# Kernel optimization log

Hardware: AMD Instinct MI355X
Metric: run time of the kernel (lower is better)

## Reference

```python
import jax, jax.numpy as jnp
import numpy as np

B, T, A, K, STEPS, E = 2, 16384, 128, 128, 16, 126


def soft_dirac_last(x):
    # softmax forward-replaced by one-hot(argmax), straight-through backward
    sm = jax.nn.softmax(x, axis=-1)
    hard = jax.nn.one_hot(jnp.argmax(x, axis=-1), x.shape[-1], dtype=x.dtype)
    return sm + jax.lax.stop_gradient(hard - sm)


def _encode(x, d_unit, atom_embeddings):
    # x: (B,1,T); d_unit: (A,K) unit-norm atoms
    rng = jnp.linspace(0.0, 1.0, T, dtype=x.dtype)
    kernel = d_unit[:, None, :]  # OIH
    pad = [(K // 2, K - 1 - K // 2)]  # SAME
    batch_ix = jnp.arange(B)

    def step(res, _):
        # dense feature map: correlation of residual with every atom
        fm = jax.lax.conv_general_dilated(
            res, kernel, window_strides=(1,), padding=pad,
            dimension_numbers=("NCH", "OIH", "NCH"))  # (B,A,T)
        flat = fm.reshape(B, A * T)
        fi = jnp.argmax(flat, axis=-1)                      # sparsify n_to_keep=1
        value = jnp.take_along_axis(flat, fi[:, None], axis=-1)  # (B,1)
        ai = fi // T
        ti = fi % T
        # position: soft_dirac over time of sparse fm summed over atoms
        pos_row = jnp.zeros((B, T), x.dtype).at[batch_ix, ti].set(value[:, 0])
        pd = soft_dirac_last(pos_row)
        position = jnp.sum(pd * rng[None, :], axis=-1, keepdims=True) * 20.0  # (B,1)
        # atom one-hot: soft_dirac over atom axis of sparse fm summed over time
        atom_row = jnp.zeros((B, A), x.dtype).at[batch_ix, ai].set(value[:, 0])
        ad = soft_dirac_last(atom_row)
        ae = ad @ atom_embeddings  # (B,E)
        emb = jnp.concatenate([position, value, ae], axis=-1)  # (B, 2+E)
        # matching-pursuit residual update: subtract value * atom at found shift
        recon = value * d_unit[ai]  # (B,K)
        buf = jnp.zeros((B, T + K), x.dtype)
        buf = jax.vmap(lambda bb, rr, tt: jax.lax.dynamic_update_slice(bb, rr, (tt,)))(buf, recon, ti)
        res = res - buf[:, None, K // 2:K // 2 + T]
        return res, emb

    res, embs = jax.lax.scan(step, x, None, length=STEPS)
    embs = jnp.transpose(embs, (1, 0, 2))  # (B, STEPS, 2+E)
    return embs, res


def _canonical_ordering(embs, proj):
    keys = embs @ proj  # (B, STEPS)
    order = jnp.argsort(keys, axis=-1)
    return jnp.take_along_axis(embs, order[:, :, None], axis=1)


def setup_inputs() -> dict:
    key = jax.random.key(0)
    ks = jax.random.split(key, 5)
    return {
        "a": jax.random.normal(ks[0], (B, 1, T), jnp.float32),
        "b": jax.random.normal(ks[1], (B, 1, T), jnp.float32),
        "d": jax.random.normal(ks[2], (A, K), jnp.float32),
        "atom_embeddings": jax.random.normal(ks[3], (A, E), jnp.float32) * 0.1,
        "ordering_proj": jax.random.normal(ks[4], (128,), jnp.float32),
    }


def reference(a, b, d, atom_embeddings, ordering_proj):
    d_unit = d / (jnp.linalg.norm(d, axis=-1, keepdims=True) + 1e-8)
    ae, a_res = _encode(a, d_unit, atom_embeddings)
    be, b_res = _encode(b, d_unit, atom_embeddings)
    ae = _canonical_ordering(ae, ordering_proj)
    be = _canonical_ordering(be, ordering_proj)
    a_norm = jnp.linalg.norm(a_res.reshape(-1, T), axis=-1)
    b_norm = jnp.linalg.norm(b_res.reshape(-1, T), axis=-1)
    return jnp.mean((ae - be) ** 2) + jnp.mean(jnp.abs(a_norm - b_norm))
```

## Files before the change

### kernel.cpp

```cpp
#include <hip/hip_runtime.h>
#include <math.h>

#define T_DIM 16384
#define A_DIM 128
#define K_DIM 128
#define N_STEPS 16
#define E_DIM 126
#define NSEQ 4

#define NPT0 512
#define NAT8 16
#define TT 256
#define NTT 64
#define HB 8192
#define RL_LEN 8319
#define SS_LEN 383
#define SPAD 16

#define PIDX(i) ((i) + ((i) >> 5))

#define NB_STEP0 (NPT0 * NSEQ)
#define NB_INC   (65 * NSEQ)
#define NB_TOTAL (NB_STEP0 + NB_INC + 1)

#define SM_U64 4448

__device__ inline unsigned long long pack_vi(float v, int fi) {
    unsigned int b = __float_as_uint(v);
    b = (b & 0x80000000u) ? ~b : (b | 0x80000000u);
    return ((unsigned long long)b << 32) | (unsigned int)(~fi);
}
__device__ inline void unpack_vi(unsigned long long p, float* v, int* fi) {
    unsigned int lo = (unsigned int)(p & 0xffffffffu);
    unsigned int b = (unsigned int)(p >> 32);
    unsigned int fb = (b & 0x80000000u) ? (b & 0x7fffffffu) : ~b;
    *v = __uint_as_float(fb);
    *fi = (int)(~lo);
}
__device__ inline unsigned long long u64max(unsigned long long a, unsigned long long b) {
    return a > b ? a : b;
}
__device__ inline unsigned long long pollu64(const unsigned long long* p) {
    unsigned long long v = __hip_atomic_load(p, __ATOMIC_RELAXED,
                                             __HIP_MEMORY_SCOPE_AGENT);
    while (v == 0ULL) {
        __builtin_amdgcn_s_sleep(1);
        v = __hip_atomic_load(p, __ATOMIC_RELAXED, __HIP_MEMORY_SCOPE_AGENT);
    }
    return v;
}

__global__ __launch_bounds__(256) void k_prep(
    const float* __restrict__ d, float* __restrict__ du,
    unsigned long long* __restrict__ arena) {
    int blk = blockIdx.x, tid = threadIdx.x;
    if (blk < 128) {
        __shared__ float s[128];
        float v = 0.0f;
        if (tid < 128) { v = d[blk * K_DIM + tid]; s[tid] = v * v; }
        __syncthreads();
        for (int off = 64; off > 0; off >>= 1) {
            if (tid < off) s[tid] += s[tid + off];
            __syncthreads();
        }
        if (tid < 128) du[blk * K_DIM + tid] = v / (sqrtf(s[0]) + 1e-8f);
    } else {
        int zb = blk - 128;
        for (int i = zb * 256 + tid; i < 31744; i += 64 * 256)
            arena[2048 + i] = 0ULL;
        if (blk == 128) {
            int* ctrl = (int*)(arena + 33792);
            if (tid < NSEQ) {
                ctrl[tid * 32] = 0;
                ((float*)ctrl)[160 + tid * 32] = 0.0f;
            }
            if (tid == 4) ctrl[128] = 0;
        }
    }
}

__device__ inline unsigned long long tile16(
    const float* __restrict__ duP, const float* __restrict__ rsh,
    int L0, int a_lo, int t_lo, int tid, unsigned long long* red4) {
    float acc[4][4];
    #pragma unroll
    for (int i = 0; i < 4; i++)
        #pragma unroll
        for (int j = 0; j < 4; j++) acc[i][j] = 0.0f;
    float r[8];
    #pragma unroll
    for (int m = 0; m < 8; m++) r[m] = rsh[PIDX(L0 + m)];
    #pragma unroll 4
    for (int k = 0; k < K_DIM; k += 4) {
        float dA[4][4];
        #pragma unroll
        for (int i = 0; i < 4; i++)
            *(float4*)dA[i] = *(const float4*)(duP + i * K_DIM + k);
        #pragma unroll
        for (int dk = 0; dk < 4; dk++) {
            #pragma unroll
            for (int i = 0; i < 4; i++) {
                float s = dA[i][dk];
                #pragma unroll
                for (int j = 0; j < 4; j++)
                    acc[i][j] = fmaf(s, r[j + dk], acc[i][j]);
            }
        }
        r[0] = r[4]; r[1] = r[5]; r[2] = r[6]; r[3] = r[7];
        #pragma unroll
        for (int m = 0; m < 4; m++) r[4 + m] = rsh[PIDX(L0 + k + 8 + m)];
    }
    float bv = -INFINITY;
    int bi = 0x7fffffff;
    #pragma unroll
    for (int i = 0; i < 4; i++) {
        int aa = a_lo + i;
        #pragma unroll
        for (int j = 0; j < 4; j++) {
            int fi = aa * T_DIM + t_lo + j;
            float v = acc[i][j];
            if (v > bv || (v == bv && fi < bi)) { bv = v; bi = fi; }
        }
    }
    #pragma unroll
    for (int off = 32; off > 0; off >>= 1) {
        float v2 = __shfl_down(bv, off);
        int   i2 = __shfl_down(bi, off);
        if (v2 > bv || (v2 == bv && i2 < bi)) { bv = v2; bi = i2; }
    }
    if ((tid & 63) == 0) red4[tid >> 6] = pack_vi(bv, bi);
    __syncthreads();
    if (tid == 0) {
        unsigned long long m = red4[0];
        #pragma unroll
        for (int w = 1; w < 4; w++) m = u64max(m, red4[w]);
        red4[0] = m;
    }
    __syncthreads();
    return red4[0];
}

__device__ inline unsigned long long tile8(
    const float* __restrict__ duP, const float* __restrict__ rsh,
    int L0, int a_lo, int t_lo, int tid, unsigned long long* red4) {
    float acc[2][4];
    #pragma unroll
    for (int i = 0; i < 2; i++)
        #pragma unroll
        for (int j = 0; j < 4; j++) acc[i][j] = 0.0f;
    float r[8];
    #pragma unroll
    for (int m = 0; m < 8; m++) r[m] = rsh[PIDX(L0 + m)];
    #pragma unroll 4
    for (int k = 0; k < K_DIM; k += 4) {
        float dA[2][4];
        #pragma unroll
        for (int i = 0; i < 2; i++)
            *(float4*)dA[i] = *(const float4*)(duP + i * K_DIM + k);
        #pragma unroll
        for (int dk = 0; dk < 4; dk++) {
            #pragma unroll
            for (int i = 0; i < 2; i++) {
                float s = dA[i][dk];
                #pragma unroll
                for (int j = 0; j < 4; j++)
                    acc[i][j] = fmaf(s, r[j + dk], acc[i][j]);
            }
        }
        r[0] = r[4]; r[1] = r[5]; r[2] = r[6]; r[3] = r[7];
        #pragma unroll
        for (int m = 0; m < 4; m++) r[4 + m] = rsh[PIDX(L0 + k + 8 + m)];
    }
    float bv = -INFINITY;
    int bi = 0x7fffffff;
    #pragma unroll
    for (int i = 0; i < 2; i++) {
        int aa = a_lo + i;
        #pragma unroll
        for (int j = 0; j < 4; j++) {
            int fi = aa * T_DIM + t_lo + j;
            float v = acc[i][j];
            if (v > bv || (v == bv && fi < bi)) { bv = v; bi = fi; }
        }
    }
    #pragma unroll
    for (int off = 32; off > 0; off >>= 1) {
        float v2 = __shfl_down(bv, off);
        int   i2 = __shfl_down(bi, off);
        if (v2 > bv || (v2 == bv && i2 < bi)) { bv = v2; bi = i2; }
    }
    if ((tid & 63) == 0) red4[tid >> 6] = pack_vi(bv, bi);
    __syncthreads();
    if (tid == 0) {
        unsigned long long m = red4[0];
        #pragma unroll
        for (int w = 1; w < 4; w++) m = u64max(m, red4[w]);
        red4[0] = m;
    }
    __syncthreads();
    return red4[0];
}

__global__ __launch_bounds__(256) void k_mega(
    const float* __restrict__ a, const float* __restrict__ b,
    const float* __restrict__ du, const float* __restrict__ ae,
    const float* __restrict__ proj, float* __restrict__ emb,
    unsigned long long* __restrict__ arena, float* __restrict__ out) {

    __shared__ unsigned long long SMEM[SM_U64];
    unsigned long long* pmax = arena;
    unsigned long long* dsl  = arena + 2048;
    unsigned long long* wsl  = arena + 32768;
    unsigned long long* w0   = arena + 33728;
    int*   cnt   = (int*)(arena + 33792);
    int*   done  = cnt + 128;
    float* norm2 = (float*)cnt + 160;

    int blk = blockIdx.x;
    int tid = threadIdx.x;

    if (blk < NB_STEP0) {
        int seq = blk >> 9;
        int idx = blk & 511;
        int a_base = (idx >> 6) * 16;
        int t0 = (idx & 63) * TT;
        float* rsh = (float*)SMEM;
        unsigned long long* pm_sh = SMEM + 256;
        unsigned long long* red4  = SMEM + 512;
        int* flag = (int*)(SMEM + 516);

        const float* x = (seq < 2 ? a : b) + (seq & 1) * T_DIM;
        for (int i = tid; i < SS_LEN; i += 256) {
            int t = t0 - 64 + i;
            rsh[PIDX(i)] = (t >= 0 && t < T_DIM) ? x[t] : 0.0f;
        }
        __syncthreads();
        int tg = tid & 63;
        int ag = __builtin_amdgcn_readfirstlane(tid >> 6);
        unsigned long long p = tile16(du + (a_base + ag * 4) * K_DIM, rsh,
                                      4 * tg, a_base + ag * 4, t0 + 4 * tg,
                                      tid, red4);
        if (tid == 0) {
            pmax[seq * NPT0 + idx] = p;
            __threadfence();
            flag[0] = (atomicAdd(&cnt[seq * 32], 1) == NPT0 - 1);
        }
        __syncthreads();
        if (!flag[0]) return;

        __threadfence();
        pm_sh[tid] = u64max(pmax[seq * NPT0 + tid], pmax[seq * NPT0 + 256 + tid]);
        __syncthreads();
        for (int off = 128; off > 0; off >>= 1) {
            if (tid < off) pm_sh[tid] = u64max(pm_sh[tid], pm_sh[tid + off]);
            __syncthreads();
        }
        float value; int fi;
        unpack_vi(pm_sh[0], &value, &fi);
        int ai = fi >> 14, ti = fi & (T_DIM - 1);
        int pos_idx = value > 0.0f ? ti : 0;
        int atom_idx = value > 0.0f ? ai : 0;
        float* e = emb + (seq * N_STEPS + 0) * 128;
        if (tid == 0) {
            e[0] = ((float)pos_idx / (float)(T_DIM - 1)) * 20.0f;
            e[1] = value;
        }
        if (tid >= 2 && tid < 2 + E_DIM) e[tid] = ae[atom_idx * E_DIM + tid - 2];
        __syncthreads();
        __threadfence();
        if (tid == 0) atomicExch(&w0[seq * SPAD], pm_sh[0]);
        return;
    }

    if (blk < NB_STEP0 + NB_INC) {
        int r = blk - NB_STEP0;
        int seq = r / 65;
        int sub = r - seq * 65;

        if (sub == 64) {
            unsigned long long* table   = SMEM;
            unsigned long long* poll_sh = SMEM + 512;
            unsigned long long* red4    = SMEM + 548;
            unsigned long long* wbc     = SMEM + 552;

            if (tid == 0) wbc[0] = pollu64(&w0[seq * SPAD]);
            __syncthreads();
            __threadfence();
            for (int i = tid; i < NPT0; i += 256) table[i] = pmax[seq * NPT0 + i];
            float v0; int fi0;
            unpack_vi(wbc[0], &v0, &fi0);
            int ti = fi0 & (T_DIM - 1);
            int lo = ti - 127; if (lo < 0) lo = 0;
            int hi = ti + 128; if (hi > T_DIM) hi = T_DIM;
            __syncthreads();

            for (int step = 1; step < N_STEPS; step++) {
                int T0 = lo >> 8, T1 = T0 + 1;
                bool hasT1 = (T1 < NTT) && (T1 * TT < hi);
                if (tid < 32) {
                    if (((tid & 1) == 0) || hasT1)
                        poll_sh[tid] = pollu64(
                            &dsl[(((step - 1) * NSEQ + seq) * 32 + tid) * SPAD]);
                }
                __syncthreads();
                if (tid < 16) {
                    int at16 = tid >> 1, ts = tid & 1;
                    if (ts == 0 || hasT1)
                        table[at16 * 64 + (ts ? T1 : T0)] =
                            u64max(poll_sh[at16 * 4 + ts], poll_sh[at16 * 4 + 2 + ts]);
                }
                __syncthreads();
                unsigned long long m = u64max(table[tid], table[tid + 256]);
                #pragma unroll
                for (int off = 32; off > 0; off >>= 1)
                    m = u64max(m, __shfl_down(m, off));
                if ((tid & 63) == 0) red4[tid >> 6] = m;
                __syncthreads();
                if (tid == 0) {
                    unsigned long long w = red4[0];
                    #pragma unroll
                    for (int j = 1; j < 4; j++) w = u64max(w, red4[j]);
                    red4[0] = w;
                    atomicExch(&wsl[((step - 1) * NSEQ + seq) * SPAD], w);
                }
                __syncthreads();
                float value; int fi;
                unpack_vi(red4[0], &value, &fi);
                int wt = fi & (T_DIM - 1);
                int wa = fi >> 14;
                int pos_idx = value > 0.0f ? wt : 0;
                int atom_idx = value > 0.0f ? wa : 0;
                float* e = emb + (seq * N_STEPS + step) * 128;
                if (tid == 0) {
                    e[0] = ((float)pos_idx / (float)(T_DIM - 1)) * 20.0f;
                    e[1] = value;
                }
                if (tid >= 2 && tid < 128) e[tid] = ae[atom_idx * E_DIM + tid - 2];
                lo = wt - 127; if (lo < 0) lo = 0;
                hi = wt + 128; if (hi > T_DIM) hi = T_DIM;
            }
            __syncthreads();
            __threadfence();
            if (tid == 0) atomicAdd(done, 1);
            return;
        }

        int atile = sub >> 2;
        int half = (sub >> 1) & 1;
        int par = sub & 1;
        int a_base = atile * 8;
        int base = half * HB;
        float* resL = (float*)SMEM;
        unsigned long long* red4 = SMEM + 4304;
        unsigned long long* wshp = SMEM + 4308;
        float* snorm = (float*)(SMEM + 4320);

        const float* x = (seq < 2 ? a : b) + (seq & 1) * T_DIM;
        for (int i = tid; i < RL_LEN; i += 256) {
            int t = base - 64 + i;
            resL[PIDX(i)] = (t >= 0 && t < T_DIM) ? x[t] : 0.0f;
        }
        if (tid == 0) wshp[0] = pollu64(&w0[seq * SPAD]);
        __syncthreads();
        float v0; int fi0;
        unpack_vi(wshp[0], &v0, &fi0);
        int ti0 = fi0 & (T_DIM - 1), ai0 = fi0 >> 14;
        if (tid < 128) {
            int t = ti0 - 64 + tid;
            if (t >= 0 && t < T_DIM) {
                int L = t - base + 64;
                if (L >= 0 && L < RL_LEN) {
                    float rr = resL[PIDX(L)];
                    resL[PIDX(L)] = __fsub_rn(rr, __fmul_rn(v0, du[ai0 * K_DIM + tid]));
                }
            }
        }
        __syncthreads();
        int lo = ti0 - 127; if (lo < 0) lo = 0;
        int hi = ti0 + 128; if (hi > T_DIM) hi = T_DIM;

        for (int step = 1; step < N_STEPS; step++) {
            int T0 = lo >> 8, T1 = T0 + 1;
            int cand = -1;
            if (((T0 & 1) == par) && ((T0 >> 5) == half)) cand = T0;
            else if (T1 < NTT && ((T1 & 1) == par) && ((T1 >> 5) == half) &&
                     T1 * TT < hi) cand = T1;

            if (cand >= 0) {
                int t0 = cand * TT;
                int tg = tid & 63;
                int ag = __builtin_amdgcn_readfirstlane(tid >> 6);
                unsigned long long p = tile8(
                    du + (a_base + ag * 2) * K_DIM, resL,
                    (t0 - base) + 4 * tg, a_base + ag * 2, t0 + 4 * tg, tid, red4);
                if (tid == 0)
                    atomicExch(&dsl[(((step - 1) * NSEQ + seq) * 32 +
                                     atile * 2 + (cand == T1 ? 1 : 0)) * SPAD], p);
            }
            if (tid == 0) wshp[0] = pollu64(&wsl[((step - 1) * NSEQ + seq) * SPAD]);
            __syncthreads();
            float value; int fi;
            unpack_vi(wshp[0], &value, &fi);
            int wt = fi & (T_DIM - 1);
            int wa = fi >> 14;
            if (tid < 128) {
                int t = wt - 64 + tid;
                if (t >= 0 && t < T_DIM) {
                    int L = t - base + 64;
                    if (L >= 0 && L < RL_LEN) {
                        float rr = resL[PIDX(L)];
                        resL[PIDX(L)] = __fsub_rn(rr, __fmul_rn(value, du[wa * K_DIM + tid]));
                    }
                }
            }
            __syncthreads();
            lo = wt - 127; if (lo < 0) lo = 0;
            hi = wt + 128; if (hi > T_DIM) hi = T_DIM;
        }

        if (atile == 0 && par == 0) {
            float s = 0.0f;
            for (int t = tid; t < HB; t += 256) {
                float v = resL[PIDX(t + 64)];
                s = fmaf(v, v, s);
            }
            snorm[tid] = s;
            __syncthreads();
            for (int off = 128; off > 0; off >>= 1) {
                if (tid < off) snorm[tid] += snorm[tid + off];
                __syncthreads();
            }
            if (tid == 0) {
                float old = atomicAdd(&norm2[seq * 32], snorm[0]);
                if (__float_as_uint(old) != 0xFFFFFFFFu)
                    atomicAdd(done, 1);
            }
        }
        return;
    }

    {
        float* keys  = (float*)SMEM;
        int*   order = (int*)(SMEM + 32);
        float* sh    = (float*)(SMEM + 64);
        float* norms = (float*)(SMEM + 192);

        if (tid == 0) {
            int c = __hip_atomic_load(done, __ATOMIC_RELAXED, __HIP_MEMORY_SCOPE_AGENT);
            while (c < 12) {
                __builtin_amdgcn_s_sleep(8);
                c = __hip_atomic_load(done, __ATOMIC_RELAXED, __HIP_MEMORY_SCOPE_AGENT);
            }
        }
        __syncthreads();
        __threadfence();

        if (tid < NSEQ)
            norms[tid] = sqrtf(__hip_atomic_load(&norm2[tid * 32], __ATOMIC_RELAXED,
                                                 __HIP_MEMORY_SCOPE_AGENT));
        if (tid < 64) {
            int seq = tid >> 4, st = tid & 15;
            const float* e = emb + (seq * N_STEPS + st) * 128;
            float kk = 0.0f;
            for (int dd = 0; dd < 128; dd++) kk = fmaf(e[dd], proj[dd], kk);
            keys[tid] = kk;
        }
        __syncthreads();
        if (tid < NSEQ) {
            int ord[N_STEPS];
            for (int i = 0; i < N_STEPS; i++) ord[i] = i;
            for (int i = 1; i < N_STEPS; i++) {
                int oi = ord[i];
                float kv = keys[tid * N_STEPS + oi];
                int j = i - 1;
                while (j >= 0 && keys[tid * N_STEPS + ord[j]] > kv) {
                    ord[j + 1] = ord[j]; j--;
                }
                ord[j + 1] = oi;
            }
            for (int i = 0; i < N_STEPS; i++) order[tid * N_STEPS + i] = ord[i];
        }
        __syncthreads();
        float s = 0.0f;
        #pragma unroll
        for (int t = 0; t < 16; t++) {
            int idx = tid + t * 256;
            int bq = idx >> 11;
            int st = (idx >> 7) & 15;
            int dd = idx & 127;
            float va = emb[((bq    ) * N_STEPS + order[bq * N_STEPS + st]) * 128 + dd];
            float vb = emb[((2 + bq) * N_STEPS + order[(2 + bq) * N_STEPS + st]) * 128 + dd];
            float df = va - vb;
            s = fmaf(df, df, s);
        }
        sh[tid] = s;
        __syncthreads();
        for (int off = 128; off > 0; off >>= 1) {
            if (tid < off) sh[tid] += sh[tid + off];
            __syncthreads();
        }
        if (tid == 0) {
            float mse = sh[0] / 4096.0f;
            float mad = 0.5f * (fabsf(norms[0] - norms[2]) + fabsf(norms[1] - norms[3]));
            out[0] = mse + mad;
        }
    }
}

extern "C" void kernel_launch(void* const* d_in, const int* in_sizes, int n_in,
                              void* d_out, int out_size, void* d_ws, size_t ws_size,
                              hipStream_t stream) {
    const float* a    = (const float*)d_in[0];
    const float* b    = (const float*)d_in[1];
    const float* d    = (const float*)d_in[2];
    const float* ae   = (const float*)d_in[3];
    const float* proj = (const float*)d_in[4];
    float* out = (float*)d_out;

    float* ws  = (float*)d_ws;
    float* du  = ws;
    float* emb = du + A_DIM * K_DIM;
    unsigned long long* arena = (unsigned long long*)(emb + NSEQ * N_STEPS * 128);

    k_prep<<<192, 256, 0, stream>>>(d, du, arena);
    k_mega<<<NB_TOTAL, 256, 0, stream>>>(a, b, du, ae, proj, emb, arena, out);
}
```

Measured before the change: 216.7 us.

## Replace persistent megakernel with Gram-matrix incremental feature-map updates

The single persistent kernel that spun on cross-block flags is replaced by five launches. The first-step correlation map is now stored in a global buffer (4×128×16384 floats). A precomputed atom Gram matrix lets each later matching-pursuit step update only the tiles near the chosen shift, with no recomputation from the residual. The residual norm is tracked analytically instead of by summing the final residual. Only four 1024-thread blocks run the 15 incremental steps, which serialises the work and adds heavy global-memory traffic. Edge positions fall back to direct dot products.

```diff
diff --git a/kernel.cpp b/kernel.cpp
--- a/kernel.cpp
+++ b/kernel.cpp
@@ -9,21 +9,17 @@
 #define NSEQ 4
 
 #define NPT0 512
-#define NAT8 16
 #define TT 256
 #define NTT 64
-#define HB 8192
-#define RL_LEN 8319
 #define SS_LEN 383
-#define SPAD 16
-
 #define PIDX(i) ((i) + ((i) >> 5))
 
-#define NB_STEP0 (NPT0 * NSEQ)
-#define NB_INC   (65 * NSEQ)
-#define NB_TOTAL (NB_STEP0 + NB_INC + 1)
-
-#define SM_U64 4448
+#define WS_DU    0
+#define WS_EMB   16384
+#define WS_NORM  24576
+#define WS_PMAX  24592
+#define WS_G     28688
+#define WS_S     (28688 + 2097152)
 
 __device__ inline unsigned long long pack_vi(float v, int fi) {
     unsigned int b = __float_as_uint(v);
@@ -40,47 +36,45 @@
 __device__ inline unsigned long long u64max(unsigned long long a, unsigned long long b) {
     return a > b ? a : b;
 }
-__device__ inline unsigned long long pollu64(const unsigned long long* p) {
-    unsigned long long v = __hip_atomic_load(p, __ATOMIC_RELAXED,
-                                             __HIP_MEMORY_SCOPE_AGENT);
-    while (v == 0ULL) {
-        __builtin_amdgcn_s_sleep(1);
-        v = __hip_atomic_load(p, __ATOMIC_RELAXED, __HIP_MEMORY_SCOPE_AGENT);
-    }
-    return v;
-}
 
 __global__ __launch_bounds__(256) void k_prep(
-    const float* __restrict__ d, float* __restrict__ du,
-    unsigned long long* __restrict__ arena) {
+    const float* __restrict__ d, float* __restrict__ du) {
     int blk = blockIdx.x, tid = threadIdx.x;
-    if (blk < 128) {
-        __shared__ float s[128];
-        float v = 0.0f;
-        if (tid < 128) { v = d[blk * K_DIM + tid]; s[tid] = v * v; }
+    __shared__ float s[128];
+    float v = 0.0f;
+    if (tid < 128) { v = d[blk * K_DIM + tid]; s[tid] = v * v; }
+    __syncthreads();
+    for (int off = 64; off > 0; off >>= 1) {
+        if (tid < off) s[tid] += s[tid + off];
         __syncthreads();
-        for (int off = 64; off > 0; off >>= 1) {
-            if (tid < off) s[tid] += s[tid + off];
-            __syncthreads();
-        }
-        if (tid < 128) du[blk * K_DIM + tid] = v / (sqrtf(s[0]) + 1e-8f);
-    } else {
-        int zb = blk - 128;
-        for (int i = zb * 256 + tid; i < 31744; i += 64 * 256)
-            arena[2048 + i] = 0ULL;
-        if (blk == 128) {
-            int* ctrl = (int*)(arena + 33792);
-            if (tid < NSEQ) {
-                ctrl[tid * 32] = 0;
-                ((float*)ctrl)[160 + tid * 32] = 0.0f;
-            }
-            if (tid == 4) ctrl[128] = 0;
-        }
-    }
-}
-
-__device__ inline unsigned long long tile16(
+    }
+    if (tid < 128) du[blk * K_DIM + tid] = v / (sqrtf(s[0]) + 1e-8f);
+}
+
+__global__ __launch_bounds__(256) void k_gram(
+    const float* __restrict__ du, float* __restrict__ G) {
+    int w = blockIdx.x >> 1, ah = blockIdx.x & 1;
+    int tid = threadIdx.x;
+    __shared__ float sw[128];
+    __shared__ float sa[64][129];
+    if (tid < 128) sw[tid] = du[w * K_DIM + tid];
+    for (int i = tid; i < 64 * 128; i += 256)
+        sa[i >> 7][i & 127] = du[(ah * 64 + (i >> 7)) * K_DIM + (i & 127)];
+    __syncthreads();
+    for (int e = 0; e < 32; e++) {
+        int idx = e * 256 + tid;
+        int dsh = idx >> 6;
+        int al = idx & 63;
+        float s = 0.0f;
+        for (int k = 0; k < 128 - dsh; k++)
+            s = fmaf(sa[al][k], sw[k + dsh], s);
+        G[w * (A_DIM * K_DIM) + (ah * 64 + al) * K_DIM + dsh] = s;
+    }
+}
+
+__device__ inline unsigned long long tile16s(
     const float* __restrict__ duP, const float* __restrict__ rsh,
+    float* __restrict__ Sp,
     int L0, int a_lo, int t_lo, int tid, unsigned long long* red4) {
     float acc[4][4];
     #pragma unroll
@@ -110,6 +104,9 @@
         #pragma unroll
         for (int m = 0; m < 4; m++) r[4 + m] = rsh[PIDX(L0 + k + 8 + m)];
     }
+    #pragma unroll
+    for (int i = 0; i < 4; i++)
+        *(float4*)(Sp + (a_lo + i) * T_DIM + t_lo) = *(const float4*)acc[i];
     float bv = -INFINITY;
     int bi = 0x7fffffff;
     #pragma unroll
@@ -133,377 +130,227 @@
     if (tid == 0) {
         unsigned long long m = red4[0];
         #pragma unroll
-        for (int w = 1; w < 4; w++) m = u64max(m, red4[w]);
+        for (int w2 = 1; w2 < 4; w2++) m = u64max(m, red4[w2]);
         red4[0] = m;
     }
     __syncthreads();
     return red4[0];
 }
 
-__device__ inline unsigned long long tile8(
-    const float* __restrict__ duP, const float* __restrict__ rsh,
-    int L0, int a_lo, int t_lo, int tid, unsigned long long* red4) {
-    float acc[2][4];
-    #pragma unroll
-    for (int i = 0; i < 2; i++)
-        #pragma unroll
-        for (int j = 0; j < 4; j++) acc[i][j] = 0.0f;
-    float r[8];
-    #pragma unroll
-    for (int m = 0; m < 8; m++) r[m] = rsh[PIDX(L0 + m)];
-    #pragma unroll 4
-    for (int k = 0; k < K_DIM; k += 4) {
-        float dA[2][4];
-        #pragma unroll
-        for (int i = 0; i < 2; i++)
-            *(float4*)dA[i] = *(const float4*)(duP + i * K_DIM + k);
-        #pragma unroll
-        for (int dk = 0; dk < 4; dk++) {
+__global__ __launch_bounds__(256) void k_step0(
+    const float* __restrict__ a, const float* __restrict__ b,
+    const float* __restrict__ du, float* __restrict__ S,
+    unsigned long long* __restrict__ pmax) {
+    __shared__ float rsh[408];
+    __shared__ unsigned long long red4[4];
+    int blk = blockIdx.x, tid = threadIdx.x;
+    int seq = blk >> 9, idx = blk & 511;
+    int a_base = (idx >> 6) * 16, t0 = (idx & 63) * TT;
+    const float* x = (seq < 2 ? a : b) + (seq & 1) * T_DIM;
+    for (int i = tid; i < SS_LEN; i += 256) {
+        int t = t0 - 64 + i;
+        rsh[PIDX(i)] = (t >= 0 && t < T_DIM) ? x[t] : 0.0f;
+    }
+    __syncthreads();
+    int tg = tid & 63;
+    int ag = __builtin_amdgcn_readfirstlane(tid >> 6);
+    unsigned long long p = tile16s(du + (a_base + ag * 4) * K_DIM, rsh,
+                                   S + seq * (A_DIM * T_DIM),
+                                   4 * tg, a_base + ag * 4, t0 + 4 * tg,
+                                   tid, red4);
+    if (tid == 0) pmax[seq * NPT0 + idx] = p;
+}
+
+__global__ __launch_bounds__(1024) void k_inc(
+    const float* __restrict__ a, const float* __restrict__ b,
+    const float* __restrict__ du, const float* __restrict__ G,
+    float* __restrict__ S, const unsigned long long* __restrict__ pmax,
+    const float* __restrict__ ae, float* __restrict__ emb,
+    float* __restrict__ normsG) {
+    __shared__ unsigned long long tm[64];
+    __shared__ unsigned long long red[16];
+    __shared__ float fred[16];
+    __shared__ unsigned long long wsh;
+    __shared__ float sn2;
+    int seq = blockIdx.x, tid = threadIdx.x;
+    const float* x = (seq < 2 ? a : b) + (seq & 1) * T_DIM;
+    float* Ss = S + seq * (A_DIM * T_DIM);
+
+    if (tid < 64) {
+        unsigned long long m = pmax[seq * NPT0 + tid];
+        #pragma unroll
+        for (int at = 1; at < 8; at++)
+            m = u64max(m, pmax[seq * NPT0 + at * 64 + tid]);
+        tm[tid] = m;
+    }
+    {
+        float s = 0.0f;
+        for (int t = tid; t < T_DIM; t += 1024) {
+            float v = x[t]; s = fmaf(v, v, s);
+        }
+        #pragma unroll
+        for (int off = 32; off > 0; off >>= 1) s += __shfl_down(s, off);
+        if ((tid & 63) == 0) fred[tid >> 6] = s;
+    }
+    __syncthreads();
+    if (tid == 0) {
+        float t = 0.0f;
+        for (int j = 0; j < 16; j++) t += fred[j];
+        sn2 = t;
+    }
+    __syncthreads();
+
+    for (int step = 0; step < N_STEPS; step++) {
+        if (tid < 64) {
+            unsigned long long m = tm[tid];
             #pragma unroll
-            for (int i = 0; i < 2; i++) {
-                float s = dA[i][dk];
+            for (int off = 32; off > 0; off >>= 1)
+                m = u64max(m, __shfl_down(m, off));
+            if (tid == 0) wsh = m;
+        }
+        __syncthreads();
+        float v; int fi;
+        unpack_vi(wsh, &v, &fi);
+        int w = fi >> 14, wt = fi & (T_DIM - 1);
+        {
+            float* e = emb + (seq * N_STEPS + step) * 128;
+            int pos_idx = v > 0.0f ? wt : 0;
+            int aidx = v > 0.0f ? w : 0;
+            if (tid == 0) {
+                e[0] = ((float)pos_idx / (float)(T_DIM - 1)) * 20.0f;
+                e[1] = v;
+            }
+            if (tid >= 2 && tid < 128) e[tid] = ae[aidx * E_DIM + tid - 2];
+        }
+        if (tid < 128) {
+            int t_res = wt + tid - 64;
+            float q = 0.0f;
+            if (t_res >= 0 && t_res < T_DIM) {
+                float dv = du[w * K_DIM + tid];
+                q = dv * dv;
+            }
+            #pragma unroll
+            for (int off = 32; off > 0; off >>= 1) q += __shfl_down(q, off);
+            if ((tid & 63) == 0) fred[8 + (tid >> 6)] = q;
+        }
+        __syncthreads();
+        if (tid == 0) {
+            float Q = fred[8] + fred[9];
+            sn2 = sn2 - v * v * (2.0f - Q);
+        }
+
+        if (step < N_STEPS - 1) {
+            int lo = wt - 127; if (lo < 0) lo = 0;
+            int hi = wt + 127; if (hi > T_DIM - 1) hi = T_DIM - 1;
+            int Tlo = lo >> 8, Thi = hi >> 8;
+            bool edge = (wt < 64) || (wt > T_DIM - 65);
+            for (int Tt = Tlo; Tt <= Thi; Tt++) {
+                unsigned long long mym = 0ULL;
+                #pragma unroll 4
+                for (int i = 0; i < 32; i++) {
+                    int idx = i * 1024 + tid;
+                    int aa = idx >> 8;
+                    int tg = (Tt << 8) + (idx & 255);
+                    float sval = Ss[aa * T_DIM + tg];
+                    int dt = tg - wt;
+                    if (dt >= -127 && dt <= 127) {
+                        float c;
+                        if (!edge) {
+                            int neg = dt < 0;
+                            int r0 = neg ? aa : w;
+                            int r1 = neg ? w : aa;
+                            int dd = neg ? -dt : dt;
+                            c = G[r0 * (A_DIM * K_DIM) + r1 * K_DIM + dd];
+                        } else {
+                            int jlo = dt > 0 ? dt : 0;
+                            { int bnd = 64 - wt; if (bnd > jlo) jlo = bnd; }
+                            int jhi = dt + 127; if (jhi > 127) jhi = 127;
+                            { int bnd = T_DIM + 63 - wt; if (bnd < jhi) jhi = bnd; }
+                            float dsum = 0.0f;
+                            for (int j = jlo; j <= jhi; j++)
+                                dsum = fmaf(du[w * K_DIM + j],
+                                            du[aa * K_DIM + j - dt], dsum);
+                            c = dsum;
+                        }
+                        sval = __fsub_rn(sval, __fmul_rn(v, c));
+                        Ss[aa * T_DIM + tg] = sval;
+                    }
+                    unsigned long long pk = pack_vi(sval, aa * T_DIM + tg);
+                    if (pk > mym) mym = pk;
+                }
                 #pragma unroll
-                for (int j = 0; j < 4; j++)
-                    acc[i][j] = fmaf(s, r[j + dk], acc[i][j]);
-            }
-        }
-        r[0] = r[4]; r[1] = r[5]; r[2] = r[6]; r[3] = r[7];
-        #pragma unroll
-        for (int m = 0; m < 4; m++) r[4 + m] = rsh[PIDX(L0 + k + 8 + m)];
-    }
-    float bv = -INFINITY;
-    int bi = 0x7fffffff;
-    #pragma unroll
-    for (int i = 0; i < 2; i++) {
-        int aa = a_lo + i;
-        #pragma unroll
-        for (int j = 0; j < 4; j++) {
-            int fi = aa * T_DIM + t_lo + j;
-            float v = acc[i][j];
-            if (v > bv || (v == bv && fi < bi)) { bv = v; bi = fi; }
-        }
-    }
-    #pragma unroll
-    for (int off = 32; off > 0; off >>= 1) {
-        float v2 = __shfl_down(bv, off);
-        int   i2 = __shfl_down(bi, off);
-        if (v2 > bv || (v2 == bv && i2 < bi)) { bv = v2; bi = i2; }
-    }
-    if ((tid & 63) == 0) red4[tid >> 6] = pack_vi(bv, bi);
-    __syncthreads();
-    if (tid == 0) {
-        unsigned long long m = red4[0];
-        #pragma unroll
-        for (int w = 1; w < 4; w++) m = u64max(m, red4[w]);
-        red4[0] = m;
-    }
-    __syncthreads();
-    return red4[0];
-}
-
-__global__ __launch_bounds__(256) void k_mega(
-    const float* __restrict__ a, const float* __restrict__ b,
-    const float* __restrict__ du, const float* __restrict__ ae,
-    const float* __restrict__ proj, float* __restrict__ emb,
-    unsigned long long* __restrict__ arena, float* __restrict__ out) {
-
-    __shared__ unsigned long long SMEM[SM_U64];
-    unsigned long long* pmax = arena;
-    unsigned long long* dsl  = arena + 2048;
-    unsigned long long* wsl  = arena + 32768;
-    unsigned long long* w0   = arena + 33728;
-    int*   cnt   = (int*)(arena + 33792);
-    int*   done  = cnt + 128;
-    float* norm2 = (float*)cnt + 160;
-
-    int blk = blockIdx.x;
-    int tid = threadIdx.x;
-
-    if (blk < NB_STEP0) {
-        int seq = blk >> 9;
-        int idx = blk & 511;
-        int a_base = (idx >> 6) * 16;
-        int t0 = (idx & 63) * TT;
-        float* rsh = (float*)SMEM;
-        unsigned long long* pm_sh = SMEM + 256;
-        unsigned long long* red4  = SMEM + 512;
-        int* flag = (int*)(SMEM + 516);
-
-        const float* x = (seq < 2 ? a : b) + (seq & 1) * T_DIM;
-        for (int i = tid; i < SS_LEN; i += 256) {
-            int t = t0 - 64 + i;
-            rsh[PIDX(i)] = (t >= 0 && t < T_DIM) ? x[t] : 0.0f;
-        }
-        __syncthreads();
-        int tg = tid & 63;
-        int ag = __builtin_amdgcn_readfirstlane(tid >> 6);
-        unsigned long long p = tile16(du + (a_base + ag * 4) * K_DIM, rsh,
-                                      4 * tg, a_base + ag * 4, t0 + 4 * tg,
-                                      tid, red4);
-        if (tid == 0) {
-            pmax[seq * NPT0 + idx] = p;
-            __threadfence();
-            flag[0] = (atomicAdd(&cnt[seq * 32], 1) == NPT0 - 1);
-        }
-        __syncthreads();
-        if (!flag[0]) return;
-
-        __threadfence();
-        pm_sh[tid] = u64max(pmax[seq * NPT0 + tid], pmax[seq * NPT0 + 256 + tid]);
-        __syncthreads();
-        for (int off = 128; off > 0; off >>= 1) {
-            if (tid < off) pm_sh[tid] = u64max(pm_sh[tid], pm_sh[tid + off]);
-            __syncthreads();
-        }
-        float value; int fi;
-        unpack_vi(pm_sh[0], &value, &fi);
-        int ai = fi >> 14, ti = fi & (T_DIM - 1);
-        int pos_idx = value > 0.0f ? ti : 0;
-        int atom_idx = value > 0.0f ? ai : 0;
-        float* e = emb + (seq * N_STEPS + 0) * 128;
-        if (tid == 0) {
-            e[0] = ((float)pos_idx / (float)(T_DIM - 1)) * 20.0f;
-            e[1] = value;
-        }
-        if (tid >= 2 && tid < 2 + E_DIM) e[tid] = ae[atom_idx * E_DIM + tid - 2];
-        __syncthreads();
-        __threadfence();
-        if (tid == 0) atomicExch(&w0[seq * SPAD], pm_sh[0]);
-        return;
-    }
-
-    if (blk < NB_STEP0 + NB_INC) {
-        int r = blk - NB_STEP0;
-        int seq = r / 65;
-        int sub = r - seq * 65;
-
-        if (sub == 64) {
-            unsigned long long* table   = SMEM;
-            unsigned long long* poll_sh = SMEM + 512;
-            unsigned long long* red4    = SMEM + 548;
-            unsigned long long* wbc     = SMEM + 552;
-
-            if (tid == 0) wbc[0] = pollu64(&w0[seq * SPAD]);
-            __syncthreads();
-            __threadfence();
-            for (int i = tid; i < NPT0; i += 256) table[i] = pmax[seq * NPT0 + i];
-            float v0; int fi0;
-            unpack_vi(wbc[0], &v0, &fi0);
-            int ti = fi0 & (T_DIM - 1);
-            int lo = ti - 127; if (lo < 0) lo = 0;
-            int hi = ti + 128; if (hi > T_DIM) hi = T_DIM;
-            __syncthreads();
-
-            for (int step = 1; step < N_STEPS; step++) {
-                int T0 = lo >> 8, T1 = T0 + 1;
-                bool hasT1 = (T1 < NTT) && (T1 * TT < hi);
-                if (tid < 32) {
-                    if (((tid & 1) == 0) || hasT1)
-                        poll_sh[tid] = pollu64(
-                            &dsl[(((step - 1) * NSEQ + seq) * 32 + tid) * SPAD]);
+                for (int off = 32; off > 0; off >>= 1)
+                    mym = u64max(mym, __shfl_down(mym, off));
+                if ((tid & 63) == 0) red[tid >> 6] = mym;
+                __syncthreads();
+                if (tid < 64) {
+                    unsigned long long m2 = (tid < 16) ? red[tid] : 0ULL;
+                    #pragma unroll
+                    for (int off = 8; off > 0; off >>= 1)
+                        m2 = u64max(m2, __shfl_down(m2, off));
+                    if (tid == 0) tm[Tt] = m2;
                 }
                 __syncthreads();
-                if (tid < 16) {
-                    int at16 = tid >> 1, ts = tid & 1;
-                    if (ts == 0 || hasT1)
-                        table[at16 * 64 + (ts ? T1 : T0)] =
-                            u64max(poll_sh[at16 * 4 + ts], poll_sh[at16 * 4 + 2 + ts]);
-                }
-                __syncthreads();
-                unsigned long long m = u64max(table[tid], table[tid + 256]);
-                #pragma unroll
-                for (int off = 32; off > 0; off >>= 1)
-                    m = u64max(m, __shfl_down(m, off));
-                if ((tid & 63) == 0) red4[tid >> 6] = m;
-                __syncthreads();
-                if (tid == 0) {
-                    unsigned long long w = red4[0];
-                    #pragma unroll
-                    for (int j = 1; j < 4; j++) w = u64max(w, red4[j]);
-                    red4[0] = w;
-                    atomicExch(&wsl[((step - 1) * NSEQ + seq) * SPAD], w);
-                }
-                __syncthreads();
-                float value; int fi;
-                unpack_vi(red4[0], &value, &fi);
-                int wt = fi & (T_DIM - 1);
-                int wa = fi >> 14;
-                int pos_idx = value > 0.0f ? wt : 0;
-                int atom_idx = value > 0.0f ? wa : 0;
-                float* e = emb + (seq * N_STEPS + step) * 128;
-                if (tid == 0) {
-                    e[0] = ((float)pos_idx / (float)(T_DIM - 1)) * 20.0f;
-                    e[1] = value;
-                }
-                if (tid >= 2 && tid < 128) e[tid] = ae[atom_idx * E_DIM + tid - 2];
-                lo = wt - 127; if (lo < 0) lo = 0;
-                hi = wt + 128; if (hi > T_DIM) hi = T_DIM;
-            }
-            __syncthreads();
-            __threadfence();
-            if (tid == 0) atomicAdd(done, 1);
-            return;
-        }
-
-        int atile = sub >> 2;
-        int half = (sub >> 1) & 1;
-        int par = sub & 1;
-        int a_base = atile * 8;
-        int base = half * HB;
-        float* resL = (float*)SMEM;
-        unsigned long long* red4 = SMEM + 4304;
-        unsigned long long* wshp = SMEM + 4308;
-        float* snorm = (float*)(SMEM + 4320);
-
-        const float* x = (seq < 2 ? a : b) + (seq & 1) * T_DIM;
-        for (int i = tid; i < RL_LEN; i += 256) {
-            int t = base - 64 + i;
-            resL[PIDX(i)] = (t >= 0 && t < T_DIM) ? x[t] : 0.0f;
-        }
-        if (tid == 0) wshp[0] = pollu64(&w0[seq * SPAD]);
+            }
+        }
+    }
+    if (tid == 0) normsG[seq] = sqrtf(sn2);
+}
+
+__global__ __launch_bounds__(256) void k_tail(
+    const float* __restrict__ emb, const float* __restrict__ normsG,
+    const float* __restrict__ proj, float* __restrict__ out) {
+    __shared__ float keys[64];
+    __shared__ int order[64];
+    __shared__ float sh[256];
+    __shared__ float norms[4];
+    int tid = threadIdx.x;
+    if (tid < NSEQ) norms[tid] = normsG[tid];
+    if (tid < 64) {
+        int seq = tid >> 4, st = tid & 15;
+        const float* e = emb + (seq * N_STEPS + st) * 128;
+        float kk = 0.0f;
+        for (int dd = 0; dd < 128; dd++) kk = fmaf(e[dd], proj[dd], kk);
+        keys[tid] = kk;
+    }
+    __syncthreads();
+    if (tid < NSEQ) {
+        int ord[N_STEPS];
+        for (int i = 0; i < N_STEPS; i++) ord[i] = i;
+        for (int i = 1; i < N_STEPS; i++) {
+            int oi = ord[i];
+            float kv = keys[tid * N_STEPS + oi];
+            int j = i - 1;
+            while (j >= 0 && keys[tid * N_STEPS + ord[j]] > kv) {
+                ord[j + 1] = ord[j]; j--;
+            }
+            ord[j + 1] = oi;
+        }
+        for (int i = 0; i < N_STEPS; i++) order[tid * N_STEPS + i] = ord[i];
+    }
+    __syncthreads();
+    float s = 0.0f;
+    #pragma unroll
+    for (int t = 0; t < 16; t++) {
+        int idx = tid + t * 256;
+        int bq = idx >> 11;
+        int st = (idx >> 7) & 15;
+        int dd = idx & 127;
+        float va = emb[((bq    ) * N_STEPS + order[bq * N_STEPS + st]) * 128 + dd];
+        float vb = emb[((2 + bq) * N_STEPS + order[(2 + bq) * N_STEPS + st]) * 128 + dd];
+        float df = va - vb;
+        s = fmaf(df, df, s);
+    }
+    sh[tid] = s;
+    __syncthreads();
+    for (int off = 128; off > 0; off >>= 1) {
+        if (tid < off) sh[tid] += sh[tid + off];
         __syncthreads();
-        float v0; int fi0;
-        unpack_vi(wshp[0], &v0, &fi0);
-        int ti0 = fi0 & (T_DIM - 1), ai0 = fi0 >> 14;
-        if (tid < 128) {
-            int t = ti0 - 64 + tid;
-            if (t >= 0 && t < T_DIM) {
-                int L = t - base + 64;
-                if (L >= 0 && L < RL_LEN) {
-                    float rr = resL[PIDX(L)];
-                    resL[PIDX(L)] = __fsub_rn(rr, __fmul_rn(v0, du[ai0 * K_DIM + tid]));
-                }
-            }
-        }
-        __syncthreads();
-        int lo = ti0 - 127; if (lo < 0) lo = 0;
-        int hi = ti0 + 128; if (hi > T_DIM) hi = T_DIM;
-
-        for (int step = 1; step < N_STEPS; step++) {
-            int T0 = lo >> 8, T1 = T0 + 1;
-            int cand = -1;
-            if (((T0 & 1) == par) && ((T0 >> 5) == half)) cand = T0;
-            else if (T1 < NTT && ((T1 & 1) == par) && ((T1 >> 5) == half) &&
-                     T1 * TT < hi) cand = T1;
-
-            if (cand >= 0) {
-                int t0 = cand * TT;
-                int tg = tid & 63;
-                int ag = __builtin_amdgcn_readfirstlane(tid >> 6);
-                unsigned long long p = tile8(
-                    du + (a_base + ag * 2) * K_DIM, resL,
-                    (t0 - base) + 4 * tg, a_base + ag * 2, t0 + 4 * tg, tid, red4);
-                if (tid == 0)
-                    atomicExch(&dsl[(((step - 1) * NSEQ + seq) * 32 +
-                                     atile * 2 + (cand == T1 ? 1 : 0)) * SPAD], p);
-            }
-            if (tid == 0) wshp[0] = pollu64(&wsl[((step - 1) * NSEQ + seq) * SPAD]);
-            __syncthreads();
-            float value; int fi;
-            unpack_vi(wshp[0], &value, &fi);
-            int wt = fi & (T_DIM - 1);
-            int wa = fi >> 14;
-            if (tid < 128) {
-                int t = wt - 64 + tid;
-                if (t >= 0 && t < T_DIM) {
-                    int L = t - base + 64;
-                    if (L >= 0 && L < RL_LEN) {
-                        float rr = resL[PIDX(L)];
-                        resL[PIDX(L)] = __fsub_rn(rr, __fmul_rn(value, du[wa * K_DIM + tid]));
-                    }
-                }
-            }
-            __syncthreads();
-            lo = wt - 127; if (lo < 0) lo = 0;
-            hi = wt + 128; if (hi > T_DIM) hi = T_DIM;
-        }
-
-        if (atile == 0 && par == 0) {
-            float s = 0.0f;
-            for (int t = tid; t < HB; t += 256) {
-                float v = resL[PIDX(t + 64)];
-                s = fmaf(v, v, s);
-            }
-            snorm[tid] = s;
-            __syncthreads();
-            for (int off = 128; off > 0; off >>= 1) {
-                if (tid < off) snorm[tid] += snorm[tid + off];
-                __syncthreads();
-            }
-            if (tid == 0) {
-                float old = atomicAdd(&norm2[seq * 32], snorm[0]);
-                if (__float_as_uint(old) != 0xFFFFFFFFu)
-                    atomicAdd(done, 1);
-            }
-        }
-        return;
-    }
-
-    {
-        float* keys  = (float*)SMEM;
-        int*   order = (int*)(SMEM + 32);
-        float* sh    = (float*)(SMEM + 64);
-        float* norms = (float*)(SMEM + 192);
-
-        if (tid == 0) {
-            int c = __hip_atomic_load(done, __ATOMIC_RELAXED, __HIP_MEMORY_SCOPE_AGENT);
-            while (c < 12) {
-                __builtin_amdgcn_s_sleep(8);
-                c = __hip_atomic_load(done, __ATOMIC_RELAXED, __HIP_MEMORY_SCOPE_AGENT);
-            }
-        }
-        __syncthreads();
-        __threadfence();
-
-        if (tid < NSEQ)
-            norms[tid] = sqrtf(__hip_atomic_load(&norm2[tid * 32], __ATOMIC_RELAXED,
-                                                 __HIP_MEMORY_SCOPE_AGENT));
-        if (tid < 64) {
-            int seq = tid >> 4, st = tid & 15;
-            const float* e = emb + (seq * N_STEPS + st) * 128;
-            float kk = 0.0f;
-            for (int dd = 0; dd < 128; dd++) kk = fmaf(e[dd], proj[dd], kk);
-            keys[tid] = kk;
-        }
-        __syncthreads();
-        if (tid < NSEQ) {
-            int ord[N_STEPS];
-            for (int i = 0; i < N_STEPS; i++) ord[i] = i;
-            for (int i = 1; i < N_STEPS; i++) {
-                int oi = ord[i];
-                float kv = keys[tid * N_STEPS + oi];
-                int j = i - 1;
-                while (j >= 0 && keys[tid * N_STEPS + ord[j]] > kv) {
-                    ord[j + 1] = ord[j]; j--;
-                }
-                ord[j + 1] = oi;
-            }
-            for (int i = 0; i < N_STEPS; i++) order[tid * N_STEPS + i] = ord[i];
-        }
-        __syncthreads();
-        float s = 0.0f;
-        #pragma unroll
-        for (int t = 0; t < 16; t++) {
-            int idx = tid + t * 256;
-            int bq = idx >> 11;
-            int st = (idx >> 7) & 15;
-            int dd = idx & 127;
-            float va = emb[((bq    ) * N_STEPS + order[bq * N_STEPS + st]) * 128 + dd];
-            float vb = emb[((2 + bq) * N_STEPS + order[(2 + bq) * N_STEPS + st]) * 128 + dd];
-            float df = va - vb;
-            s = fmaf(df, df, s);
-        }
-        sh[tid] = s;
-        __syncthreads();
-        for (int off = 128; off > 0; off >>= 1) {
-            if (tid < off) sh[tid] += sh[tid + off];
-            __syncthreads();
-        }
-        if (tid == 0) {
-            float mse = sh[0] / 4096.0f;
-            float mad = 0.5f * (fabsf(norms[0] - norms[2]) + fabsf(norms[1] - norms[3]));
-            out[0] = mse + mad;
-        }
+    }
+    if (tid == 0) {
+        float mse = sh[0] / 4096.0f;
+        float mad = 0.5f * (fabsf(norms[0] - norms[2]) + fabsf(norms[1] - norms[3]));
+        out[0] = mse + mad;
     }
 }
 
@@ -517,11 +364,17 @@
     const float* proj = (const float*)d_in[4];
     float* out = (float*)d_out;
 
-    float* ws  = (float*)d_ws;
-    float* du  = ws;
-    float* emb = du + A_DIM * K_DIM;
-    unsigned long long* arena = (unsigned long long*)(emb + NSEQ * N_STEPS * 128);
-
-    k_prep<<<192, 256, 0, stream>>>(d, du, arena);
-    k_mega<<<NB_TOTAL, 256, 0, stream>>>(a, b, du, ae, proj, emb, arena, out);
-}
+    float* ws     = (float*)d_ws;
+    float* du     = ws + WS_DU;
+    float* emb    = ws + WS_EMB;
+    float* normsG = ws + WS_NORM;
+    unsigned long long* pmax = (unsigned long long*)(ws + WS_PMAX);
+    float* G      = ws + WS_G;
+    float* S      = ws + WS_S;
+
+    k_prep <<<128,  256, 0, stream>>>(d, du);
+    k_gram <<<256,  256, 0, stream>>>(du, G);
+    k_step0<<<2048, 256, 0, stream>>>(a, b, du, S, pmax);
+    k_inc  <<<4,   1024, 0, stream>>>(a, b, du, G, S, pmax, ae, emb, normsG);
+    k_tail <<<1,    256, 0, stream>>>(emb, normsG, proj, out);
+}
```

Measured after the change: 541.6 us. 2.5x slower.
